# Performance work log

Hardware: AMD Instinct MI355X
Metric: run time of the kernel (lower is better)

Reference implementation:

```python
import jax, jax.numpy as jnp
import numpy as np

B, T_Q, T_C = 4, 2048, 2048
Q_DIM = C_DIM = H_DIM = OUT_DIM = 1024
N_HEADS = 16
D = H_DIM // N_HEADS


def setup_inputs() -> dict:
    key = jax.random.key(0)
    ks = jax.random.split(key, 10)
    s_q = 1.0 / np.sqrt(Q_DIM)
    s_c = 1.0 / np.sqrt(C_DIM)
    s_h = 1.0 / np.sqrt(H_DIM)
    return {
        "query": jax.random.normal(ks[0], (B, T_Q, Q_DIM), jnp.float32),
        "context": jax.random.normal(ks[1], (B, T_C, C_DIM), jnp.float32),
        "Wq": jax.random.uniform(ks[2], (Q_DIM, H_DIM), jnp.float32, -s_q, s_q),
        "bq": jax.random.uniform(ks[3], (H_DIM,), jnp.float32, -s_q, s_q),
        "Wk": jax.random.uniform(ks[4], (C_DIM, H_DIM), jnp.float32, -s_c, s_c),
        "bk": jax.random.uniform(ks[5], (H_DIM,), jnp.float32, -s_c, s_c),
        "Wv": jax.random.uniform(ks[6], (C_DIM, H_DIM), jnp.float32, -s_c, s_c),
        "bv": jax.random.uniform(ks[7], (H_DIM,), jnp.float32, -s_c, s_c),
        "Wo": jax.random.uniform(ks[8], (H_DIM, OUT_DIM), jnp.float32, -s_h, s_h),
        "bo": jax.random.uniform(ks[9], (OUT_DIM,), jnp.float32, -s_h, s_h),
    }


def reference(query, context, Wq, bq, Wk, bk, Wv, bv, Wo, bo):
    Bq, Tq, _ = query.shape
    _, Tc, _ = context.shape
    # project and split heads: [B, H, T, D]
    q = (query @ Wq + bq).reshape(Bq, Tq, N_HEADS, D).transpose(0, 2, 1, 3)
    k = (context @ Wk + bk).reshape(Bq, Tc, N_HEADS, D).transpose(0, 2, 1, 3)
    v = (context @ Wv + bv).reshape(Bq, Tc, N_HEADS, D).transpose(0, 2, 1, 3)
    scores = jnp.einsum("bhqd,bhkd->bhqk", q, k) / jnp.sqrt(jnp.float32(D))
    probs = jax.nn.softmax(scores, axis=-1)
    attn = jnp.einsum("bhqk,bhkd->bhqd", probs, v)  # dropout p=0 -> identity
    attn = attn.transpose(0, 2, 1, 3).reshape(Bq, Tq, N_HEADS * D)
    return attn @ Wo + bo
```

## Files before the change

### kernel.cpp

```cpp
#include <hip/hip_runtime.h>
#include <hip/hip_bf16.h>
#include <cstdint>

typedef __attribute__((ext_vector_type(8))) short short8;
typedef __attribute__((ext_vector_type(4))) short short4_t;
typedef __attribute__((ext_vector_type(4))) float f32x4;

#define MFMA16(a, b, c) __builtin_amdgcn_mfma_f32_16x16x32_bf16(a, b, c, 0, 0, 0)

__device__ __forceinline__ short f2b(float f) {
    union { float fp; unsigned u; } un; un.fp = f;
    unsigned r = un.u + 0x7fffu + ((un.u >> 16) & 1u);
    return (short)(r >> 16);
}

#if __has_builtin(__builtin_amdgcn_cvt_pk_bf16_f32)
__device__ __forceinline__ unsigned pk_bf16(float a, float b) {
    auto r = __builtin_amdgcn_cvt_pk_bf16_f32(a, b);
    unsigned u; __builtin_memcpy(&u, &r, 4); return u;
}
#else
__device__ __forceinline__ unsigned pk_bf16(float a, float b) {
    return (unsigned)(unsigned short)f2b(a) | ((unsigned)(unsigned short)f2b(b) << 16);
}
#endif

union pk8_u { unsigned u4[4]; short8 s8; };
union cat8_u { short4_t s4[2]; short8 s8; };

typedef const __attribute__((address_space(1))) unsigned g_as1;
typedef __attribute__((address_space(3))) unsigned l_as3;
__device__ __forceinline__ void gll16(const ushort* g, ushort* l) {
    __builtin_amdgcn_global_load_lds((g_as1*)g, (l_as3*)l, 16, 0, 0);
}

__global__ __launch_bounds__(256) void in_cvt_kernel(
    const float* __restrict__ q, const float* __restrict__ c,
    ushort* __restrict__ qb, ushort* __restrict__ cb)
{
    const float* src = blockIdx.y ? c : q;
    ushort* dst = blockIdx.y ? cb : qb;
    size_t i = ((size_t)blockIdx.x * 256 + threadIdx.x) * 8;
    float4 v0 = *(const float4*)&src[i];
    float4 v1 = *(const float4*)&src[i + 4];
    uint4 o;
    o.x = pk_bf16(v0.x, v0.y); o.y = pk_bf16(v0.z, v0.w);
    o.z = pk_bf16(v1.x, v1.y); o.w = pk_bf16(v1.z, v1.w);
    *(uint4*)&dst[i] = o;
}

__global__ __launch_bounds__(256) void wt_cvt_kernel(
    const float* __restrict__ Wq, const float* __restrict__ Wk,
    const float* __restrict__ Wv, const float* __restrict__ Wo,
    ushort* __restrict__ wt)
{
    __shared__ float Ts[64 * 65];
    const int z = blockIdx.z;
    const float* W = (z == 0) ? Wq : (z == 1) ? Wk : (z == 2) ? Wv : Wo;
    ushort* WT = wt + (size_t)z * (1024 * 1024);
    const int n0 = blockIdx.x * 64, k0 = blockIdx.y * 64;
    const int tid = threadIdx.x;

#pragma unroll
    for (int rr = 0; rr < 4; ++rr) {
        int u = tid + rr * 256;
        int r = u >> 4, c = (u & 15) * 4;
        float4 v = *(const float4*)&W[(size_t)(k0 + r) * 1024 + n0 + c];
        Ts[r * 65 + c + 0] = v.x; Ts[r * 65 + c + 1] = v.y;
        Ts[r * 65 + c + 2] = v.z; Ts[r * 65 + c + 3] = v.w;
    }
    __syncthreads();
#pragma unroll
    for (int rr = 0; rr < 4; ++rr) {
        int u = tid + rr * 256;
        int rn = u >> 4, ck = (u & 15) * 4;
        short4_t o;
        o[0] = f2b(Ts[(ck + 0) * 65 + rn]);
        o[1] = f2b(Ts[(ck + 1) * 65 + rn]);
        o[2] = f2b(Ts[(ck + 2) * 65 + rn]);
        o[3] = f2b(Ts[(ck + 3) * 65 + rn]);
        *(short4_t*)&WT[(size_t)(n0 + rn) * 1024 + k0 + ck] = o;
    }
}

template <int MODE>
__global__ __launch_bounds__(256) void gemm_kernel(
    const ushort* __restrict__ Ag, const ushort* __restrict__ BT,
    const float* __restrict__ bias, void* __restrict__ Outp, float scale)
{
    __shared__ ushort As[128 * 64];
    __shared__ ushort Bs[128 * 64];
    const int tid = threadIdx.x;
    const int w = tid >> 6, lane = tid & 63;
    const int ln = tid & 15, quad = (tid >> 4) & 3;
    const int wm = w >> 1, wn = w & 1;
    const int m0 = blockIdx.y * 128, n0 = blockIdx.x * 128;

    int offA[4], offB[4], lseg[4];
#pragma unroll
    for (int rr = 0; rr < 4; ++rr) {
        int idx = (rr * 4 + w) * 64 + lane;
        int r = idx >> 3, cst = idx & 7, csrc = cst ^ (r & 7);
        offA[rr] = (m0 + r) * 1024 + csrc * 8;
        offB[rr] = (n0 + r) * 1024 + csrc * 8;
        lseg[rr] = (rr * 4 + w) * 512;
    }

    f32x4 acc[4][4] = {};

    for (int kk = 0; kk < 1024; kk += 64) {
        __syncthreads();
#pragma unroll
        for (int rr = 0; rr < 4; ++rr)
            gll16(&Ag[(size_t)(offA[rr] + kk)], &As[lseg[rr]]);
#pragma unroll
        for (int rr = 0; rr < 4; ++rr)
            gll16(&BT[(size_t)(offB[rr] + kk)], &Bs[lseg[rr]]);
        __syncthreads();

#pragma unroll
        for (int ks = 0; ks < 2; ++ks) {
            short8 af[4], bfr[4];
#pragma unroll
            for (int i = 0; i < 4; ++i)
                af[i] = *(const short8*)&As[(wm * 64 + i * 16 + ln) * 64 +
                                            ((ks * 4 + quad) ^ (ln & 7)) * 8];
#pragma unroll
            for (int j = 0; j < 4; ++j)
                bfr[j] = *(const short8*)&Bs[(wn * 64 + j * 16 + ln) * 64 +
                                             ((ks * 4 + quad) ^ (ln & 7)) * 8];
#pragma unroll
            for (int i = 0; i < 4; ++i)
#pragma unroll
                for (int j = 0; j < 4; ++j)
                    acc[i][j] = MFMA16(af[i], bfr[j], acc[i][j]);
        }
    }

#pragma unroll
    for (int j = 0; j < 4; ++j) {
        int n = n0 + wn * 64 + j * 16 + ln;
        float bv = bias[n];
#pragma unroll
        for (int i = 0; i < 4; ++i) {
            int mb = m0 + wm * 64 + i * 16 + quad * 4;
            if (MODE == 3) {
                float* Out = (float*)Outp;
#pragma unroll
                for (int r = 0; r < 4; ++r)
                    Out[(size_t)(mb + r) * 1024 + n] = acc[i][j][r] + bv;
            } else {
                ushort* Out = (ushort*)Outp;
                int h = n >> 6, d = n & 63;
#pragma unroll
                for (int r = 0; r < 4; ++r) {
                    int m = mb + r, b = m >> 11, t = m & 2047;
                    Out[(((size_t)(b * 16 + h) * 2048 + t) << 6) + d] =
                        (ushort)f2b((acc[i][j][r] + bv) * scale);
                }
            }
        }
    }
}

__global__ __launch_bounds__(256) void kv_kernel(
    const ushort* __restrict__ Cb, const ushort* __restrict__ WTk,
    const ushort* __restrict__ WTv,
    const float* __restrict__ bk, const float* __restrict__ bv,
    ushort* __restrict__ Kw, ushort* __restrict__ Vtw)
{
    __shared__ ushort As[128 * 64];
    __shared__ ushort Bs[128 * 64];
    const int tid = threadIdx.x;
    const int w = tid >> 6, lane = tid & 63;
    const int ln = tid & 15, quad = (tid >> 4) & 3;
    const int wm = w >> 1, wn = w & 1;
    const int z = blockIdx.x >> 3;
    const int n0 = (blockIdx.x & 7) * 128;
    const int m0 = blockIdx.y * 128;
    const ushort* BT = z ? WTv : WTk;

    int offA[4], offB[4], lseg[4];
#pragma unroll
    for (int rr = 0; rr < 4; ++rr) {
        int idx = (rr * 4 + w) * 64 + lane;
        int r = idx >> 3, cst = idx & 7, csrc = cst ^ (r & 7);
        offA[rr] = (m0 + r) * 1024 + csrc * 8;
        offB[rr] = (n0 + r) * 1024 + csrc * 8;
        lseg[rr] = (rr * 4 + w) * 512;
    }

    f32x4 acc[4][4] = {};

    for (int kk = 0; kk < 1024; kk += 64) {
        __syncthreads();
#pragma unroll
        for (int rr = 0; rr < 4; ++rr)
            gll16(&Cb[(size_t)(offA[rr] + kk)], &As[lseg[rr]]);
#pragma unroll
        for (int rr = 0; rr < 4; ++rr)
            gll16(&BT[(size_t)(offB[rr] + kk)], &Bs[lseg[rr]]);
        __syncthreads();

#pragma unroll
        for (int ks = 0; ks < 2; ++ks) {
            short8 af[4], bfr[4];
#pragma unroll
            for (int i = 0; i < 4; ++i)
                af[i] = *(const short8*)&As[(wm * 64 + i * 16 + ln) * 64 +
                                            ((ks * 4 + quad) ^ (ln & 7)) * 8];
#pragma unroll
            for (int j = 0; j < 4; ++j)
                bfr[j] = *(const short8*)&Bs[(wn * 64 + j * 16 + ln) * 64 +
                                             ((ks * 4 + quad) ^ (ln & 7)) * 8];
#pragma unroll
            for (int i = 0; i < 4; ++i)
#pragma unroll
                for (int j = 0; j < 4; ++j)
                    acc[i][j] = MFMA16(af[i], bfr[j], acc[i][j]);
        }
    }

#pragma unroll
    for (int j = 0; j < 4; ++j) {
        int n = n0 + wn * 64 + j * 16 + ln;
        int h = n >> 6, d = n & 63;
        if (z == 0) {
            float bvv = bk[n];
#pragma unroll
            for (int i = 0; i < 4; ++i) {
                int mb = m0 + wm * 64 + i * 16 + quad * 4;
#pragma unroll
                for (int r = 0; r < 4; ++r) {
                    int m = mb + r, b = m >> 11, t = m & 2047;
                    Kw[(((size_t)(b * 16 + h) * 2048 + t) << 6) + d] =
                        (ushort)f2b(acc[i][j][r] + bvv);
                }
            }
        } else {
            float bvv = bv[n];
#pragma unroll
            for (int i = 0; i < 4; ++i) {
                int mb = m0 + wm * 64 + i * 16 + quad * 4;
                int b = mb >> 11, t = mb & 2047;
                short4_t o;
                o[0] = f2b(acc[i][j][0] + bvv); o[1] = f2b(acc[i][j][1] + bvv);
                o[2] = f2b(acc[i][j][2] + bvv); o[3] = f2b(acc[i][j][3] + bvv);
                *(short4_t*)&Vtw[(((size_t)((b * 16 + h) * 64 + d)) << 11) + t] = o;
            }
        }
    }
}

__global__ __launch_bounds__(256, 4) void attn_kernel(
    const ushort* __restrict__ Qw, const ushort* __restrict__ Kw,
    const ushort* __restrict__ Vtw, ushort* __restrict__ attn)
{
    __shared__ ushort Ks[2][4096];
    __shared__ ushort Vts[2][4096];

    const int tid = threadIdx.x;
    const int w = tid >> 6, lane = tid & 63;
    const int ln = tid & 15, quad = (tid >> 4) & 3;
    const int id = blockIdx.x;
    const int qt = (id >> 3) & 15;
    const int bh = (id & 7) | ((id >> 7) << 3);
    const int b = bh >> 4, h = bh & 15;

    const ushort* Qg = Qw + (size_t)bh * 131072 + (size_t)qt * 8192;
    const ushort* Kg = Kw + (size_t)bh * 131072;
    const ushort* Vg = Vtw + (size_t)bh * 131072;

    short8 bq[2][2];
#pragma unroll
    for (int qs = 0; qs < 2; ++qs)
#pragma unroll
        for (int ks = 0; ks < 2; ++ks)
            bq[qs][ks] = *(const short8*)&Qg[(w * 32 + qs * 16 + ln) * 64 + ks * 32 + quad * 8];

    int offK[2], offV[2], lseg[2];
#pragma unroll
    for (int rr = 0; rr < 2; ++rr) {
        int idx = (rr * 4 + w) * 64 + lane;
        int r = idx >> 3, cst = idx & 7, csrc = cst ^ (r & 7);
        offK[rr] = r * 64 + csrc * 8;
        offV[rr] = r * 2048 + csrc * 8;
        lseg[rr] = (rr * 4 + w) * 512;
    }

    const short8 ones8 = {(short)0x3F80, (short)0x3F80, (short)0x3F80, (short)0x3F80,
                          (short)0x3F80, (short)0x3F80, (short)0x3F80, (short)0x3F80};

    f32x4 Of[2][4] = {};
    f32x4 lac[2] = {};

#pragma unroll
    for (int rr = 0; rr < 2; ++rr) gll16(&Kg[offK[rr]], &Ks[0][lseg[rr]]);
#pragma unroll
    for (int rr = 0; rr < 2; ++rr) gll16(&Vg[offV[rr]], &Vts[0][lseg[rr]]);
    __syncthreads();

    auto body = [&](int kt, const ushort* Kc, const ushort* Vc,
                    ushort* Kn, ushort* Vn) {
        if (kt < 31) {
#pragma unroll
            for (int rr = 0; rr < 2; ++rr)
                gll16(&Kg[(kt + 1) * 4096 + offK[rr]], &Kn[lseg[rr]]);
#pragma unroll
            for (int rr = 0; rr < 2; ++rr)
                gll16(&Vg[(kt + 1) * 64 + offV[rr]], &Vn[lseg[rr]]);
        }

        short8 pf8[2][2];
#pragma unroll
        for (int c = 0; c < 2; ++c) {
            f32x4 s[2][2];
#pragma unroll
            for (int kb = 0; kb < 2; ++kb) {
                int kv = 2 * c + kb;
                short8 a0 = *(const short8*)&Kc[(kv * 16 + ln) * 64 + (quad ^ (ln & 7)) * 8];
                short8 a1 = *(const short8*)&Kc[(kv * 16 + ln) * 64 + ((4 + quad) ^ (ln & 7)) * 8];
#pragma unroll
                for (int qs = 0; qs < 2; ++qs) {
                    f32x4 t = {};
                    t = MFMA16(a0, bq[qs][0], t);
                    t = MFMA16(a1, bq[qs][1], t);
                    s[kb][qs] = t;
                }
            }
#pragma unroll
            for (int qs = 0; qs < 2; ++qs) {
                pk8_u pu;
                pu.u4[0] = pk_bf16(__builtin_amdgcn_exp2f(s[0][qs][0]),
                                   __builtin_amdgcn_exp2f(s[0][qs][1]));
                pu.u4[1] = pk_bf16(__builtin_amdgcn_exp2f(s[0][qs][2]),
                                   __builtin_amdgcn_exp2f(s[0][qs][3]));
                pu.u4[2] = pk_bf16(__builtin_amdgcn_exp2f(s[1][qs][0]),
                                   __builtin_amdgcn_exp2f(s[1][qs][1]));
                pu.u4[3] = pk_bf16(__builtin_amdgcn_exp2f(s[1][qs][2]),
                                   __builtin_amdgcn_exp2f(s[1][qs][3]));
                pf8[c][qs] = pu.s8;
                lac[qs] = MFMA16(ones8, pu.s8, lac[qs]);
            }
        }

#pragma unroll
        for (int c = 0; c < 2; ++c) {
#pragma unroll
            for (int ds = 0; ds < 4; ++ds) {
                const ushort* vrow = &Vc[(ds * 16 + ln) * 64];
                cat8_u av;
                av.s4[0] = *(const short4_t*)&vrow[(((4 * c + (quad >> 1)) ^ (ln & 7)) * 8) + (quad & 1) * 4];
                av.s4[1] = *(const short4_t*)&vrow[(((4 * c + 2 + (quad >> 1)) ^ (ln & 7)) * 8) + (quad & 1) * 4];
#pragma unroll
                for (int qs = 0; qs < 2; ++qs)
                    Of[qs][ds] = MFMA16(av.s8, pf8[c][qs], Of[qs][ds]);
            }
        }

        __syncthreads();
    };

    for (int kt = 0; kt < 32; kt += 2) {
        body(kt,     Ks[0], Vts[0], Ks[1], Vts[1]);
        body(kt + 1, Ks[1], Vts[1], Ks[0], Vts[0]);
    }

#pragma unroll
    for (int qs = 0; qs < 2; ++qs) {
        float inv = __builtin_amdgcn_rcpf(lac[qs][0]);
        int t = qt * 128 + w * 32 + qs * 16 + ln;
        size_t base = ((size_t)(b * 2048 + t) << 10) + h * 64;
#pragma unroll
        for (int ds = 0; ds < 4; ++ds) {
            uint2 o;
            o.x = pk_bf16(Of[qs][ds][0] * inv, Of[qs][ds][1] * inv);
            o.y = pk_bf16(Of[qs][ds][2] * inv, Of[qs][ds][3] * inv);
            *(uint2*)&attn[base + ds * 16 + quad * 4] = o;
        }
    }
}

extern "C" void kernel_launch(void* const* d_in, const int* in_sizes, int n_in,
                              void* d_out, int out_size, void* d_ws, size_t ws_size,
                              hipStream_t stream)
{
    const float* query   = (const float*)d_in[0];
    const float* context = (const float*)d_in[1];
    const float* Wq = (const float*)d_in[2];
    const float* bq = (const float*)d_in[3];
    const float* Wk = (const float*)d_in[4];
    const float* bk = (const float*)d_in[5];
    const float* Wv = (const float*)d_in[6];
    const float* bv = (const float*)d_in[7];
    const float* Wo = (const float*)d_in[8];
    const float* bo = (const float*)d_in[9];

    char* ws = (char*)d_ws;
    ushort* WT  = (ushort*)ws;
    ushort* Qb  = (ushort*)(ws + 8388608);
    ushort* Qw  = (ushort*)(ws + 25165824);
    ushort* Kw  = (ushort*)(ws + 41943040);
    ushort* Vtw = (ushort*)(ws + 58720256);
    ushort* Aw  = Qb;
    ushort* Cb  = (ushort*)d_out;

    const float SCALE = 0.18033688011112042f;

    in_cvt_kernel<<<dim3(4096, 2), 256, 0, stream>>>(query, context, Qb, Cb);
    wt_cvt_kernel<<<dim3(16, 16, 4), 256, 0, stream>>>(Wq, Wk, Wv, Wo, WT);
    gemm_kernel<0><<<dim3(8, 64), 256, 0, stream>>>(Qb, WT + 0 * 1048576, bq, Qw, SCALE);
    kv_kernel<<<dim3(16, 64), 256, 0, stream>>>(Cb, WT + 1 * 1048576,
                                                WT + 2 * 1048576, bk, bv, Kw, Vtw);
    attn_kernel<<<dim3(1024), 256, 0, stream>>>(Qw, Kw, Vtw, Aw);
    gemm_kernel<3><<<dim3(8, 64), 256, 0, stream>>>(Aw, WT + 3 * 1048576, bo,
                                                    (float*)d_out, 1.0f);
}
```

Measured before the change: 320.2 us.

## Merge conversion and projection launches, restructure attention loop with MFMA priority

The input and weight conversion kernels become one launch. The Q projection and the K/V projection GEMMs become a single 1536-block launch that picks its operand and output mode from the block id. Together these cut launch count and the tail gaps between kernels. The attention inner loop now interleaves QK, exp and PV per chunk, batches the LDS loads before each MFMA group, and wraps the MFMA groups in s_setprio to favour matrix issue over other waves. This may raise register pressure and adds branching in the merged kernels.

```diff
diff --git a/kernel.cpp b/kernel.cpp
--- a/kernel.cpp
+++ b/kernel.cpp
@@ -34,46 +34,49 @@
     __builtin_amdgcn_global_load_lds((g_as1*)g, (l_as3*)l, 16, 0, 0);
 }
 
-__global__ __launch_bounds__(256) void in_cvt_kernel(
+__global__ __launch_bounds__(256) void cvt_all_kernel(
     const float* __restrict__ q, const float* __restrict__ c,
-    ushort* __restrict__ qb, ushort* __restrict__ cb)
-{
-    const float* src = blockIdx.y ? c : q;
-    ushort* dst = blockIdx.y ? cb : qb;
-    size_t i = ((size_t)blockIdx.x * 256 + threadIdx.x) * 8;
-    float4 v0 = *(const float4*)&src[i];
-    float4 v1 = *(const float4*)&src[i + 4];
-    uint4 o;
-    o.x = pk_bf16(v0.x, v0.y); o.y = pk_bf16(v0.z, v0.w);
-    o.z = pk_bf16(v1.x, v1.y); o.w = pk_bf16(v1.z, v1.w);
-    *(uint4*)&dst[i] = o;
-}
-
-__global__ __launch_bounds__(256) void wt_cvt_kernel(
+    ushort* __restrict__ qb, ushort* __restrict__ cb,
     const float* __restrict__ Wq, const float* __restrict__ Wk,
     const float* __restrict__ Wv, const float* __restrict__ Wo,
     ushort* __restrict__ wt)
 {
     __shared__ float Ts[64 * 65];
-    const int z = blockIdx.z;
+    const int id = blockIdx.x;
+    const int tid = threadIdx.x;
+
+    if (id < 8192) {
+        const float* src = (id >= 4096) ? c : q;
+        ushort* dst = (id >= 4096) ? cb : qb;
+        size_t i = ((size_t)(id & 4095) * 256 + tid) * 8;
+        float4 v0 = *(const float4*)&src[i];
+        float4 v1 = *(const float4*)&src[i + 4];
+        uint4 o;
+        o.x = pk_bf16(v0.x, v0.y); o.y = pk_bf16(v0.z, v0.w);
+        o.z = pk_bf16(v1.x, v1.y); o.w = pk_bf16(v1.z, v1.w);
+        *(uint4*)&dst[i] = o;
+        return;
+    }
+
+    const int u = id - 8192;
+    const int z = u >> 8;
     const float* W = (z == 0) ? Wq : (z == 1) ? Wk : (z == 2) ? Wv : Wo;
     ushort* WT = wt + (size_t)z * (1024 * 1024);
-    const int n0 = blockIdx.x * 64, k0 = blockIdx.y * 64;
-    const int tid = threadIdx.x;
+    const int n0 = (u & 15) * 64, k0 = ((u >> 4) & 15) * 64;
 
 #pragma unroll
     for (int rr = 0; rr < 4; ++rr) {
-        int u = tid + rr * 256;
-        int r = u >> 4, c = (u & 15) * 4;
-        float4 v = *(const float4*)&W[(size_t)(k0 + r) * 1024 + n0 + c];
-        Ts[r * 65 + c + 0] = v.x; Ts[r * 65 + c + 1] = v.y;
-        Ts[r * 65 + c + 2] = v.z; Ts[r * 65 + c + 3] = v.w;
+        int uu = tid + rr * 256;
+        int r = uu >> 4, cc = (uu & 15) * 4;
+        float4 v = *(const float4*)&W[(size_t)(k0 + r) * 1024 + n0 + cc];
+        Ts[r * 65 + cc + 0] = v.x; Ts[r * 65 + cc + 1] = v.y;
+        Ts[r * 65 + cc + 2] = v.z; Ts[r * 65 + cc + 3] = v.w;
     }
     __syncthreads();
 #pragma unroll
     for (int rr = 0; rr < 4; ++rr) {
-        int u = tid + rr * 256;
-        int rn = u >> 4, ck = (u & 15) * 4;
+        int uu = tid + rr * 256;
+        int rn = uu >> 4, ck = (uu & 15) * 4;
         short4_t o;
         o[0] = f2b(Ts[(ck + 0) * 65 + rn]);
         o[1] = f2b(Ts[(ck + 1) * 65 + rn]);
@@ -83,10 +86,123 @@
     }
 }
 
-template <int MODE>
-__global__ __launch_bounds__(256) void gemm_kernel(
+__global__ __launch_bounds__(256) void proj_kernel(
+    const ushort* __restrict__ Qb, const ushort* __restrict__ Cb,
+    const ushort* __restrict__ WTbase,
+    const float* __restrict__ biasq, const float* __restrict__ biask,
+    const float* __restrict__ biasv,
+    ushort* __restrict__ Qw, ushort* __restrict__ Kw, ushort* __restrict__ Vtw,
+    float scale)
+{
+    __shared__ ushort As[128 * 64];
+    __shared__ ushort Bs[128 * 64];
+    const int tid = threadIdx.x;
+    const int w = tid >> 6, lane = tid & 63;
+    const int ln = tid & 15, quad = (tid >> 4) & 3;
+    const int wm = w >> 1, wn = w & 1;
+
+    const int id = blockIdx.x;
+    int m0, n0, mode;
+    const ushort* Ag;
+    const ushort* BT;
+    if (id < 1024) {
+        mode = (id & 15) >> 3;
+        n0 = (id & 7) * 128;
+        m0 = (id >> 4) * 128;
+        Ag = Cb;
+        BT = WTbase + (size_t)(1 + mode) * 1048576;
+    } else {
+        int u = id - 1024;
+        mode = 2;
+        n0 = (u & 7) * 128;
+        m0 = (u >> 3) * 128;
+        Ag = Qb;
+        BT = WTbase;
+    }
+
+    int offA[4], offB[4], lseg[4];
+#pragma unroll
+    for (int rr = 0; rr < 4; ++rr) {
+        int idx = (rr * 4 + w) * 64 + lane;
+        int r = idx >> 3, cst = idx & 7, csrc = cst ^ (r & 7);
+        offA[rr] = (m0 + r) * 1024 + csrc * 8;
+        offB[rr] = (n0 + r) * 1024 + csrc * 8;
+        lseg[rr] = (rr * 4 + w) * 512;
+    }
+
+    f32x4 acc[4][4] = {};
+
+    for (int kk = 0; kk < 1024; kk += 64) {
+        __syncthreads();
+#pragma unroll
+        for (int rr = 0; rr < 4; ++rr)
+            gll16(&Ag[(size_t)(offA[rr] + kk)], &As[lseg[rr]]);
+#pragma unroll
+        for (int rr = 0; rr < 4; ++rr)
+            gll16(&BT[(size_t)(offB[rr] + kk)], &Bs[lseg[rr]]);
+        __syncthreads();
+
+#pragma unroll
+        for (int ks = 0; ks < 2; ++ks) {
+            short8 af[4], bfr[4];
+#pragma unroll
+            for (int i = 0; i < 4; ++i)
+                af[i] = *(const short8*)&As[(wm * 64 + i * 16 + ln) * 64 +
+                                            ((ks * 4 + quad) ^ (ln & 7)) * 8];
+#pragma unroll
+            for (int j = 0; j < 4; ++j)
+                bfr[j] = *(const short8*)&Bs[(wn * 64 + j * 16 + ln) * 64 +
+                                             ((ks * 4 + quad) ^ (ln & 7)) * 8];
+#pragma unroll
+            for (int i = 0; i < 4; ++i)
+#pragma unroll
+                for (int j = 0; j < 4; ++j)
+                    acc[i][j] = MFMA16(af[i], bfr[j], acc[i][j]);
+        }
+    }
+
+    if (mode == 1) {
+#pragma unroll
+        for (int j = 0; j < 4; ++j) {
+            int n = n0 + wn * 64 + j * 16 + ln;
+            int h = n >> 6, d = n & 63;
+            float bvv = biasv[n];
+#pragma unroll
+            for (int i = 0; i < 4; ++i) {
+                int mb = m0 + wm * 64 + i * 16 + quad * 4;
+                int b = mb >> 11, t = mb & 2047;
+                short4_t o;
+                o[0] = f2b(acc[i][j][0] + bvv); o[1] = f2b(acc[i][j][1] + bvv);
+                o[2] = f2b(acc[i][j][2] + bvv); o[3] = f2b(acc[i][j][3] + bvv);
+                *(short4_t*)&Vtw[(((size_t)((b * 16 + h) * 64 + d)) << 11) + t] = o;
+            }
+        }
+    } else {
+        ushort* Out = (mode == 2) ? Qw : Kw;
+        const float* bias = (mode == 2) ? biasq : biask;
+        float sc = (mode == 2) ? scale : 1.0f;
+#pragma unroll
+        for (int j = 0; j < 4; ++j) {
+            int n = n0 + wn * 64 + j * 16 + ln;
+            int h = n >> 6, d = n & 63;
+            float bvv = bias[n];
+#pragma unroll
+            for (int i = 0; i < 4; ++i) {
+                int mb = m0 + wm * 64 + i * 16 + quad * 4;
+#pragma unroll
+                for (int r = 0; r < 4; ++r) {
+                    int m = mb + r, b = m >> 11, t = m & 2047;
+                    Out[(((size_t)(b * 16 + h) * 2048 + t) << 6) + d] =
+                        (ushort)f2b((acc[i][j][r] + bvv) * sc);
+                }
+            }
+        }
+    }
+}
+
+__global__ __launch_bounds__(256) void gemm_o_kernel(
     const ushort* __restrict__ Ag, const ushort* __restrict__ BT,
-    const float* __restrict__ bias, void* __restrict__ Outp, float scale)
+    const float* __restrict__ bias, float* __restrict__ Out)
 {
     __shared__ ushort As[128 * 64];
     __shared__ ushort Bs[128 * 64];
@@ -144,110 +260,9 @@
 #pragma unroll
         for (int i = 0; i < 4; ++i) {
             int mb = m0 + wm * 64 + i * 16 + quad * 4;
-            if (MODE == 3) {
-                float* Out = (float*)Outp;
-#pragma unroll
-                for (int r = 0; r < 4; ++r)
-                    Out[(size_t)(mb + r) * 1024 + n] = acc[i][j][r] + bv;
-            } else {
-                ushort* Out = (ushort*)Outp;
-                int h = n >> 6, d = n & 63;
-#pragma unroll
-                for (int r = 0; r < 4; ++r) {
-                    int m = mb + r, b = m >> 11, t = m & 2047;
-                    Out[(((size_t)(b * 16 + h) * 2048 + t) << 6) + d] =
-                        (ushort)f2b((acc[i][j][r] + bv) * scale);
-                }
-            }
-        }
-    }
-}
-
-__global__ __launch_bounds__(256) void kv_kernel(
-    const ushort* __restrict__ Cb, const ushort* __restrict__ WTk,
-    const ushort* __restrict__ WTv,
-    const float* __restrict__ bk, const float* __restrict__ bv,
-    ushort* __restrict__ Kw, ushort* __restrict__ Vtw)
-{
-    __shared__ ushort As[128 * 64];
-    __shared__ ushort Bs[128 * 64];
-    const int tid = threadIdx.x;
-    const int w = tid >> 6, lane = tid & 63;
-    const int ln = tid & 15, quad = (tid >> 4) & 3;
-    const int wm = w >> 1, wn = w & 1;
-    const int z = blockIdx.x >> 3;
-    const int n0 = (blockIdx.x & 7) * 128;
-    const int m0 = blockIdx.y * 128;
-    const ushort* BT = z ? WTv : WTk;
-
-    int offA[4], offB[4], lseg[4];
-#pragma unroll
-    for (int rr = 0; rr < 4; ++rr) {
-        int idx = (rr * 4 + w) * 64 + lane;
-        int r = idx >> 3, cst = idx & 7, csrc = cst ^ (r & 7);
-        offA[rr] = (m0 + r) * 1024 + csrc * 8;
-        offB[rr] = (n0 + r) * 1024 + csrc * 8;
-        lseg[rr] = (rr * 4 + w) * 512;
-    }
-
-    f32x4 acc[4][4] = {};
-
-    for (int kk = 0; kk < 1024; kk += 64) {
-        __syncthreads();
-#pragma unroll
-        for (int rr = 0; rr < 4; ++rr)
-            gll16(&Cb[(size_t)(offA[rr] + kk)], &As[lseg[rr]]);
-#pragma unroll
-        for (int rr = 0; rr < 4; ++rr)
-            gll16(&BT[(size_t)(offB[rr] + kk)], &Bs[lseg[rr]]);
-        __syncthreads();
-
-#pragma unroll
-        for (int ks = 0; ks < 2; ++ks) {
-            short8 af[4], bfr[4];
-#pragma unroll
-            for (int i = 0; i < 4; ++i)
-                af[i] = *(const short8*)&As[(wm * 64 + i * 16 + ln) * 64 +
-                                            ((ks * 4 + quad) ^ (ln & 7)) * 8];
-#pragma unroll
-            for (int j = 0; j < 4; ++j)
-                bfr[j] = *(const short8*)&Bs[(wn * 64 + j * 16 + ln) * 64 +
-                                             ((ks * 4 + quad) ^ (ln & 7)) * 8];
-#pragma unroll
-            for (int i = 0; i < 4; ++i)
-#pragma unroll
-                for (int j = 0; j < 4; ++j)
-                    acc[i][j] = MFMA16(af[i], bfr[j], acc[i][j]);
-        }
-    }
-
-#pragma unroll
-    for (int j = 0; j < 4; ++j) {
-        int n = n0 + wn * 64 + j * 16 + ln;
-        int h = n >> 6, d = n & 63;
-        if (z == 0) {
-            float bvv = bk[n];
-#pragma unroll
-            for (int i = 0; i < 4; ++i) {
-                int mb = m0 + wm * 64 + i * 16 + quad * 4;
-#pragma unroll
-                for (int r = 0; r < 4; ++r) {
-                    int m = mb + r, b = m >> 11, t = m & 2047;
-                    Kw[(((size_t)(b * 16 + h) * 2048 + t) << 6) + d] =
-                        (ushort)f2b(acc[i][j][r] + bvv);
-                }
-            }
-        } else {
-            float bvv = bv[n];
-#pragma unroll
-            for (int i = 0; i < 4; ++i) {
-                int mb = m0 + wm * 64 + i * 16 + quad * 4;
-                int b = mb >> 11, t = mb & 2047;
-                short4_t o;
-                o[0] = f2b(acc[i][j][0] + bvv); o[1] = f2b(acc[i][j][1] + bvv);
-                o[2] = f2b(acc[i][j][2] + bvv); o[3] = f2b(acc[i][j][3] + bvv);
-                *(short4_t*)&Vtw[(((size_t)((b * 16 + h) * 64 + d)) << 11) + t] = o;
-            }
+#pragma unroll
+            for (int r = 0; r < 4; ++r)
+                Out[(size_t)(mb + r) * 1024 + n] = acc[i][j][r] + bv;
         }
     }
 }
@@ -311,23 +326,29 @@
                 gll16(&Vg[(kt + 1) * 64 + offV[rr]], &Vn[lseg[rr]]);
         }
 
-        short8 pf8[2][2];
 #pragma unroll
         for (int c = 0; c < 2; ++c) {
-            f32x4 s[2][2];
+            short8 a0[2], a1[2];
 #pragma unroll
             for (int kb = 0; kb < 2; ++kb) {
                 int kv = 2 * c + kb;
-                short8 a0 = *(const short8*)&Kc[(kv * 16 + ln) * 64 + (quad ^ (ln & 7)) * 8];
-                short8 a1 = *(const short8*)&Kc[(kv * 16 + ln) * 64 + ((4 + quad) ^ (ln & 7)) * 8];
+                a0[kb] = *(const short8*)&Kc[(kv * 16 + ln) * 64 + (quad ^ (ln & 7)) * 8];
+                a1[kb] = *(const short8*)&Kc[(kv * 16 + ln) * 64 + ((4 + quad) ^ (ln & 7)) * 8];
+            }
+            f32x4 s[2][2];
+            __builtin_amdgcn_s_setprio(1);
+#pragma unroll
+            for (int kb = 0; kb < 2; ++kb)
 #pragma unroll
                 for (int qs = 0; qs < 2; ++qs) {
                     f32x4 t = {};
-                    t = MFMA16(a0, bq[qs][0], t);
-                    t = MFMA16(a1, bq[qs][1], t);
+                    t = MFMA16(a0[kb], bq[qs][0], t);
+                    t = MFMA16(a1[kb], bq[qs][1], t);
                     s[kb][qs] = t;
                 }
-            }
+            __builtin_amdgcn_s_setprio(0);
+
+            short8 pf8[2];
 #pragma unroll
             for (int qs = 0; qs < 2; ++qs) {
                 pk8_u pu;
@@ -339,23 +360,24 @@
                                    __builtin_amdgcn_exp2f(s[1][qs][1]));
                 pu.u4[3] = pk_bf16(__builtin_amdgcn_exp2f(s[1][qs][2]),
                                    __builtin_amdgcn_exp2f(s[1][qs][3]));
-                pf8[c][qs] = pu.s8;
+                pf8[qs] = pu.s8;
                 lac[qs] = MFMA16(ones8, pu.s8, lac[qs]);
             }
-        }
-
-#pragma unroll
-        for (int c = 0; c < 2; ++c) {
+
+            cat8_u av[4];
 #pragma unroll
             for (int ds = 0; ds < 4; ++ds) {
                 const ushort* vrow = &Vc[(ds * 16 + ln) * 64];
-                cat8_u av;
-                av.s4[0] = *(const short4_t*)&vrow[(((4 * c + (quad >> 1)) ^ (ln & 7)) * 8) + (quad & 1) * 4];
-                av.s4[1] = *(const short4_t*)&vrow[(((4 * c + 2 + (quad >> 1)) ^ (ln & 7)) * 8) + (quad & 1) * 4];
+                av[ds].s4[0] = *(const short4_t*)&vrow[(((4 * c + (quad >> 1)) ^ (ln & 7)) * 8) + (quad & 1) * 4];
+                av[ds].s4[1] = *(const short4_t*)&vrow[(((4 * c + 2 + (quad >> 1)) ^ (ln & 7)) * 8) + (quad & 1) * 4];
+            }
+            __builtin_amdgcn_s_setprio(1);
+#pragma unroll
+            for (int ds = 0; ds < 4; ++ds)
 #pragma unroll
                 for (int qs = 0; qs < 2; ++qs)
-                    Of[qs][ds] = MFMA16(av.s8, pf8[c][qs], Of[qs][ds]);
-            }
+                    Of[qs][ds] = MFMA16(av[ds].s8, pf8[qs], Of[qs][ds]);
+            __builtin_amdgcn_s_setprio(0);
         }
 
         __syncthreads();
@@ -407,12 +429,11 @@
 
     const float SCALE = 0.18033688011112042f;
 
-    in_cvt_kernel<<<dim3(4096, 2), 256, 0, stream>>>(query, context, Qb, Cb);
-    wt_cvt_kernel<<<dim3(16, 16, 4), 256, 0, stream>>>(Wq, Wk, Wv, Wo, WT);
-    gemm_kernel<0><<<dim3(8, 64), 256, 0, stream>>>(Qb, WT + 0 * 1048576, bq, Qw, SCALE);
-    kv_kernel<<<dim3(16, 64), 256, 0, stream>>>(Cb, WT + 1 * 1048576,
-                                                WT + 2 * 1048576, bk, bv, Kw, Vtw);
+    cvt_all_kernel<<<dim3(9216), 256, 0, stream>>>(query, context, Qb, Cb,
+                                                   Wq, Wk, Wv, Wo, WT);
+    proj_kernel<<<dim3(1536), 256, 0, stream>>>(Qb, Cb, WT, bq, bk, bv,
+                                                Qw, Kw, Vtw, SCALE);
     attn_kernel<<<dim3(1024), 256, 0, stream>>>(Qw, Kw, Vtw, Aw);
-    gemm_kernel<3><<<dim3(8, 64), 256, 0, stream>>>(Aw, WT + 3 * 1048576, bo,
-                                                    (float*)d_out, 1.0f);
-}
+    gemm_o_kernel<<<dim3(8, 64), 256, 0, stream>>>(Aw, WT + 3 * 1048576, bo,
+                                                   (float*)d_out);
+}
```

Result: faster. 312.6 us (-2.4%).
